# Optimization experiments

Measured on AMD Instinct MI355X. Metric: run time of the kernel, lower is better.

Reference implementation:

```python
import jax, jax.numpy as jnp
import numpy as np
from jax import lax

NUM_INPUTS = 1024
NUM_OUTPUTS = 1024
NUM_LAYERS = 32          # 1 first + (NUM_LAYERS-1) middle + 1 last, per torch __init__
N = 4096                 # num_neurons_per_layer
W = 65536                # parallel bit-array width


def _nand_layer(x, idx, mask):
    # x: [num_in, W] bool; idx: [num_out, 2] int; mask: [num_out] bool
    g = x[idx]                       # [num_out, 2, W] gather
    out = g[:, 0, :] & g[:, 1, :]    # bitwise AND
    return jnp.where(mask[:, None], ~out, out)  # conditional NOT


def setup_inputs() -> dict:
    key = jax.random.key(0)
    k = jax.random.split(key, 7)
    n_mid = NUM_LAYERS - 1
    return {
        "input_bitarrays": jax.random.bernoulli(k[0], 0.5, (NUM_INPUTS, W)),
        "idx_first": jax.random.randint(k[1], (N, 2), 0, NUM_INPUTS, dtype=jnp.int64 if jax.config.jax_enable_x64 else jnp.int32),
        "mask_first": jax.random.bernoulli(k[2], 0.5, (N,)),
        "idx_mid": jax.random.randint(k[3], (n_mid, N, 2), 0, N, dtype=jnp.int64 if jax.config.jax_enable_x64 else jnp.int32),
        "mask_mid": jax.random.bernoulli(k[4], 0.5, (n_mid, N)),
        "idx_last": jax.random.randint(k[5], (NUM_OUTPUTS, 2), 0, N, dtype=jnp.int64 if jax.config.jax_enable_x64 else jnp.int32),
        "mask_last": jax.random.bernoulli(k[6], 0.5, (NUM_OUTPUTS,)),
    }


def reference(input_bitarrays, idx_first, mask_first, idx_mid, mask_mid, idx_last, mask_last):
    x = _nand_layer(input_bitarrays, idx_first, mask_first)

    def step(carry, params):
        idx, mask = params
        return _nand_layer(carry, idx, mask), None

    x, _ = lax.scan(step, x, (idx_mid, mask_mid))
    return _nand_layer(x, idx_last, mask_last)
```

## Files before the change

### kernel.cpp

```cpp
#include <hip/hip_runtime.h>
#include <stdint.h>

#define NINPUTS   1024
#define NOUTPUTS  1024
#define NMID      31
#define NN        4096
#define W         65536
#define CHUNK     128
#define WPN       4
#define NCHUNKS   (W / CHUNK)
#define GRID      256
#define CPW       (NCHUNKS / GRID)
#define THREADS   1024
#define NPAIRS    16
#define TBL_BYTES ((size_t)NPAIRS * NN * 16)

__global__ void build_tbl_kernel(const int*      __restrict__ idx_first,
                                 const uint32_t* __restrict__ mask_first,
                                 const int*      __restrict__ idx_mid,
                                 const uint32_t* __restrict__ mask_mid,
                                 uint4*          __restrict__ tbl)
{
    const int tid = blockIdx.x * blockDim.x + threadIdx.x;
    const int F = tid >> 12;
    const int n = tid & (NN - 1);

    const int*      i1;
    const uint32_t* m1;
    if (F == 0) { i1 = idx_first; m1 = mask_first; }
    else        { i1 = idx_mid + (size_t)(2 * F - 1) * NN * 2;
                  m1 = mask_mid + (size_t)(2 * F - 1) * NN; }
    const int*      i2 = idx_mid + (size_t)(2 * F) * NN * 2;
    const uint32_t* m2 = mask_mid + (size_t)(2 * F) * NN;

    const int j = i2[2 * n];
    const int k = i2[2 * n + 1];
    uint4 e;
    e.x = (uint32_t)(i1[2 * j]     * 16) | (m1[j] ? 0x80000000u : 0u);
    e.y = (uint32_t)(i1[2 * j + 1] * 16);
    e.z = (uint32_t)(i1[2 * k]     * 16) | (m1[k] ? 0x80000000u : 0u);
    e.w = (uint32_t)(i1[2 * k + 1] * 16) | (m2[n] ? 0x80000000u : 0u);
    tbl[(size_t)F * NN + n] = e;
}

__global__ __launch_bounds__(THREADS, 4)
void nand_fused_kernel(const uint32_t* __restrict__ in,
                       const uint4*    __restrict__ tbl,
                       const int*      __restrict__ idx_last,
                       const uint32_t* __restrict__ mask_last,
                       uint32_t*       __restrict__ out)
{
    __shared__ uint32_t lds[40960];
    uint32_t* P = lds;
    uint32_t* X = lds + 4096;
    uint32_t* Y = lds + 20480;
    uint32_t* R = lds + 36864;

    const int t      = threadIdx.x;
    const int l      = t & 63;
    const int wv     = t >> 6;
    const int lane32 = l & 31;
    const int half   = l >> 5;
    const int shift  = half ? 32 : 0;
    const int bcol   = blockIdx.x * (CPW * CHUNK);

    #pragma unroll 4
    for (int s = 0; s < 32; ++s) {
        const int r = s * 32 + wv * 2 + half;
        const uint4 v = *(const uint4*)(in + (size_t)r * W + bcol + lane32 * 4);
        const unsigned long long b0 = __ballot(v.x != 0u);
        const unsigned long long b1 = __ballot(v.y != 0u);
        const unsigned long long b2 = __ballot(v.z != 0u);
        const unsigned long long b3 = __ballot(v.w != 0u);
        if (lane32 == 0) {
            uint4 w;
            w.x = (uint32_t)(b0 >> shift);
            w.y = (uint32_t)(b1 >> shift);
            w.z = (uint32_t)(b2 >> shift);
            w.w = (uint32_t)(b3 >> shift);
            *(uint4*)&P[r * WPN] = w;
        }
    }
    __syncthreads();

    for (int i = 0; i < CPW; ++i) {
        const int c0n = bcol + (i + 1) * CHUNK;
        const int c0p = bcol + (i - 1) * CHUNK;
        const bool do_pack   = (i + 1 < CPW);
        const bool do_unpack = (i > 0);

        uint4 tc[4], tn[4];
        #pragma unroll
        for (int k = 0; k < 4; ++k) tc[k] = tbl[k * THREADS + t];

        for (int F = 0; F <= 16; ++F) {
            uint4 pv0 = {0,0,0,0}, pv1 = {0,0,0,0};
            int pr0 = 0, pr1 = 0;
            if (do_pack && F >= 1) {
                pr0 = (F - 1) * 64 + wv * 2 + half;
                pr1 = pr0 + 32;
                pv0 = *(const uint4*)(in + (size_t)pr0 * W + c0n + lane32 * 4);
                pv1 = *(const uint4*)(in + (size_t)pr1 * W + c0n + lane32 * 4);
            }
            if (F <= 14) {
                #pragma unroll
                for (int k = 0; k < 4; ++k)
                    tn[k] = tbl[(size_t)(F + 1) * NN + k * THREADS + t];
            }

            if (F <= 15) {
                const uint32_t* src = (F == 0) ? P : ((F & 1) ? X : Y);
                uint32_t*       dst = (F & 1) ? Y : X;
                #pragma unroll
                for (int k = 0; k < 4; ++k) {
                    const int n = k * THREADS + t;
                    const uint4 e = tc[k];
                    const uint32_t xm1 = (uint32_t)((int32_t)e.x >> 31);
                    const uint32_t xm2 = (uint32_t)((int32_t)e.z >> 31);
                    const uint32_t xm3 = (uint32_t)((int32_t)e.w >> 31);
                    const uint4 a = *(const uint4*)((const char*)src + (e.x & 0xFFFFu));
                    const uint4 b = *(const uint4*)((const char*)src + e.y);
                    const uint4 c = *(const uint4*)((const char*)src + (e.z & 0xFFFFu));
                    const uint4 d = *(const uint4*)((const char*)src + (e.w & 0xFFFFu));
                    uint4 r;
                    r.x = (((a.x & b.x) ^ xm1) & ((c.x & d.x) ^ xm2)) ^ xm3;
                    r.y = (((a.y & b.y) ^ xm1) & ((c.y & d.y) ^ xm2)) ^ xm3;
                    r.z = (((a.z & b.z) ^ xm1) & ((c.z & d.z) ^ xm2)) ^ xm3;
                    r.w = (((a.w & b.w) ^ xm1) & ((c.w & d.w) ^ xm2)) ^ xm3;
                    *(uint4*)&dst[n * WPN] = r;
                }
            } else {
                const int n = t;
                const int2 ij = ((const int2*)idx_last)[n];
                const uint32_t xm = mask_last[n] ? 0xFFFFFFFFu : 0u;
                const uint4 a = *(const uint4*)&Y[ij.x * WPN];
                const uint4 b = *(const uint4*)&Y[ij.y * WPN];
                uint4 r;
                r.x = (a.x & b.x) ^ xm;  r.y = (a.y & b.y) ^ xm;
                r.z = (a.z & b.z) ^ xm;  r.w = (a.w & b.w) ^ xm;
                *(uint4*)&R[n * WPN] = r;
            }

            if (do_unpack && F <= 15) {
                #pragma unroll
                for (int s = 0; s < 2; ++s) {
                    const int r = F * 64 + s * 32 + wv * 2 + half;
                    const uint4 w4 = *(const uint4*)&R[r * WPN];
                    uint4 v;
                    v.x = (w4.x >> lane32) & 1u;
                    v.y = (w4.y >> lane32) & 1u;
                    v.z = (w4.z >> lane32) & 1u;
                    v.w = (w4.w >> lane32) & 1u;
                    *(uint4*)(out + (size_t)r * W + c0p + lane32 * 4) = v;
                }
            }

            if (do_pack && F >= 1) {
                {
                    const unsigned long long b0 = __ballot(pv0.x != 0u);
                    const unsigned long long b1 = __ballot(pv0.y != 0u);
                    const unsigned long long b2 = __ballot(pv0.z != 0u);
                    const unsigned long long b3 = __ballot(pv0.w != 0u);
                    if (lane32 == 0) {
                        uint4 w;
                        w.x = (uint32_t)(b0 >> shift);
                        w.y = (uint32_t)(b1 >> shift);
                        w.z = (uint32_t)(b2 >> shift);
                        w.w = (uint32_t)(b3 >> shift);
                        *(uint4*)&P[pr0 * WPN] = w;
                    }
                }
                {
                    const unsigned long long b0 = __ballot(pv1.x != 0u);
                    const unsigned long long b1 = __ballot(pv1.y != 0u);
                    const unsigned long long b2 = __ballot(pv1.z != 0u);
                    const unsigned long long b3 = __ballot(pv1.w != 0u);
                    if (lane32 == 0) {
                        uint4 w;
                        w.x = (uint32_t)(b0 >> shift);
                        w.y = (uint32_t)(b1 >> shift);
                        w.z = (uint32_t)(b2 >> shift);
                        w.w = (uint32_t)(b3 >> shift);
                        *(uint4*)&P[pr1 * WPN] = w;
                    }
                }
            }

            if (F <= 14) {
                #pragma unroll
                for (int k = 0; k < 4; ++k) tc[k] = tn[k];
            }
            __syncthreads();
        }
    }

    {
        const int c0l = bcol + (CPW - 1) * CHUNK;
        #pragma unroll 4
        for (int s = 0; s < 32; ++s) {
            const int r = s * 32 + wv * 2 + half;
            const uint4 w4 = *(const uint4*)&R[r * WPN];
            uint4 v;
            v.x = (w4.x >> lane32) & 1u;
            v.y = (w4.y >> lane32) & 1u;
            v.z = (w4.z >> lane32) & 1u;
            v.w = (w4.w >> lane32) & 1u;
            *(uint4*)(out + (size_t)r * W + c0l + lane32 * 4) = v;
        }
    }
}

__global__ __launch_bounds__(THREADS, 4)
void nand_pipe128_kernel(const uint32_t* __restrict__ in,
                         const int*      __restrict__ idx_first,
                         const uint32_t* __restrict__ mask_first,
                         const int*      __restrict__ idx_mid,
                         const uint32_t* __restrict__ mask_mid,
                         const int*      __restrict__ idx_last,
                         const uint32_t* __restrict__ mask_last,
                         uint32_t*       __restrict__ out)
{
    __shared__ uint32_t lds[40960];
    uint32_t* P = lds;
    uint32_t* X = lds + 4096;
    uint32_t* Y = lds + 20480;
    uint32_t* R = lds + 36864;

    const int t      = threadIdx.x;
    const int l      = t & 63;
    const int wv     = t >> 6;
    const int lane32 = l & 31;
    const int half   = l >> 5;
    const int shift  = half ? 32 : 0;
    const int bcol   = blockIdx.x * (CPW * CHUNK);

    #pragma unroll 4
    for (int s = 0; s < 32; ++s) {
        const int r = s * 32 + wv * 2 + half;
        const uint4 v = *(const uint4*)(in + (size_t)r * W + bcol + lane32 * 4);
        const unsigned long long b0 = __ballot(v.x != 0u);
        const unsigned long long b1 = __ballot(v.y != 0u);
        const unsigned long long b2 = __ballot(v.z != 0u);
        const unsigned long long b3 = __ballot(v.w != 0u);
        if (lane32 == 0) {
            uint4 w;
            w.x = (uint32_t)(b0 >> shift);  w.y = (uint32_t)(b1 >> shift);
            w.z = (uint32_t)(b2 >> shift);  w.w = (uint32_t)(b3 >> shift);
            *(uint4*)&P[r * WPN] = w;
        }
    }
    __syncthreads();

    for (int i = 0; i < CPW; ++i) {
        const int c0n = bcol + (i + 1) * CHUNK;
        const int c0p = bcol + (i - 1) * CHUNK;
        const bool do_pack   = (i + 1 < CPW);
        const bool do_unpack = (i > 0);

        for (int L = 0; L <= 32; ++L) {
            uint4 pv = {0, 0, 0, 0};
            int   pr = 0;
            if (do_pack && L >= 1) {
                pr = (L - 1) * 32 + wv * 2 + half;
                pv = *(const uint4*)(in + (size_t)pr * W + c0n + lane32 * 4);
            }
            if (L == 0) {
                #pragma unroll
                for (int k = 0; k < NN / THREADS; ++k) {
                    const int n = k * THREADS + t;
                    const int2 ij = ((const int2*)idx_first)[n];
                    const uint32_t xm = mask_first[n] ? 0xFFFFFFFFu : 0u;
                    const uint4 a = *(const uint4*)&P[ij.x * WPN];
                    const uint4 b = *(const uint4*)&P[ij.y * WPN];
                    uint4 r;
                    r.x = (a.x & b.x) ^ xm;  r.y = (a.y & b.y) ^ xm;
                    r.z = (a.z & b.z) ^ xm;  r.w = (a.w & b.w) ^ xm;
                    *(uint4*)&X[n * WPN] = r;
                }
            } else if (L <= 31) {
                const int*      idxL = idx_mid + (size_t)(L - 1) * NN * 2;
                const uint32_t* mL   = mask_mid + (size_t)(L - 1) * NN;
                const uint32_t* src  = (L & 1) ? X : Y;
                uint32_t*       dst  = (L & 1) ? Y : X;
                #pragma unroll
                for (int k = 0; k < NN / THREADS; ++k) {
                    const int n = k * THREADS + t;
                    const int2 ij = ((const int2*)idxL)[n];
                    const uint32_t xm = mL[n] ? 0xFFFFFFFFu : 0u;
                    const uint4 a = *(const uint4*)&src[ij.x * WPN];
                    const uint4 b = *(const uint4*)&src[ij.y * WPN];
                    uint4 r;
                    r.x = (a.x & b.x) ^ xm;  r.y = (a.y & b.y) ^ xm;
                    r.z = (a.z & b.z) ^ xm;  r.w = (a.w & b.w) ^ xm;
                    *(uint4*)&dst[n * WPN] = r;
                }
            } else {
                const int n = t;
                const int2 ij = ((const int2*)idx_last)[n];
                const uint32_t xm = mask_last[n] ? 0xFFFFFFFFu : 0u;
                const uint4 a = *(const uint4*)&Y[ij.x * WPN];
                const uint4 b = *(const uint4*)&Y[ij.y * WPN];
                uint4 r;
                r.x = (a.x & b.x) ^ xm;  r.y = (a.y & b.y) ^ xm;
                r.z = (a.z & b.z) ^ xm;  r.w = (a.w & b.w) ^ xm;
                *(uint4*)&R[n * WPN] = r;
            }
            if (do_unpack && L <= 31) {
                const int r = L * 32 + wv * 2 + half;
                const uint4 w4 = *(const uint4*)&R[r * WPN];
                uint4 v;
                v.x = (w4.x >> lane32) & 1u;  v.y = (w4.y >> lane32) & 1u;
                v.z = (w4.z >> lane32) & 1u;  v.w = (w4.w >> lane32) & 1u;
                *(uint4*)(out + (size_t)r * W + c0p + lane32 * 4) = v;
            }
            if (do_pack && L >= 1) {
                const unsigned long long b0 = __ballot(pv.x != 0u);
                const unsigned long long b1 = __ballot(pv.y != 0u);
                const unsigned long long b2 = __ballot(pv.z != 0u);
                const unsigned long long b3 = __ballot(pv.w != 0u);
                if (lane32 == 0) {
                    uint4 w;
                    w.x = (uint32_t)(b0 >> shift);  w.y = (uint32_t)(b1 >> shift);
                    w.z = (uint32_t)(b2 >> shift);  w.w = (uint32_t)(b3 >> shift);
                    *(uint4*)&P[pr * WPN] = w;
                }
            }
            __syncthreads();
        }
    }
    {
        const int c0l = bcol + (CPW - 1) * CHUNK;
        #pragma unroll 4
        for (int s = 0; s < 32; ++s) {
            const int r = s * 32 + wv * 2 + half;
            const uint4 w4 = *(const uint4*)&R[r * WPN];
            uint4 v;
            v.x = (w4.x >> lane32) & 1u;  v.y = (w4.y >> lane32) & 1u;
            v.z = (w4.z >> lane32) & 1u;  v.w = (w4.w >> lane32) & 1u;
            *(uint4*)(out + (size_t)r * W + c0l + lane32 * 4) = v;
        }
    }
}

extern "C" void kernel_launch(void* const* d_in, const int* in_sizes, int n_in,
                              void* d_out, int out_size, void* d_ws, size_t ws_size,
                              hipStream_t stream) {
    const uint32_t* in         = (const uint32_t*)d_in[0];
    const int*      idx_first  = (const int*)d_in[1];
    const uint32_t* mask_first = (const uint32_t*)d_in[2];
    const int*      idx_mid    = (const int*)d_in[3];
    const uint32_t* mask_mid   = (const uint32_t*)d_in[4];
    const int*      idx_last   = (const int*)d_in[5];
    const uint32_t* mask_last  = (const uint32_t*)d_in[6];
    uint32_t*       out        = (uint32_t*)d_out;

    if (ws_size >= TBL_BYTES) {
        uint4* tbl = (uint4*)d_ws;
        build_tbl_kernel<<<(NPAIRS * NN) / 256, 256, 0, stream>>>(
            idx_first, mask_first, idx_mid, mask_mid, tbl);
        nand_fused_kernel<<<GRID, THREADS, 0, stream>>>(
            in, tbl, idx_last, mask_last, out);
    } else {
        nand_pipe128_kernel<<<GRID, THREADS, 0, stream>>>(
            in, idx_first, mask_first, idx_mid, mask_mid, idx_last, mask_last, out);
    }
}
```

Before: 158.5 us.

## Sort fused gate table by LDS bank key to cut bank conflicts

The table-building kernel now counting-sorts the fused two-layer gate entries within each layer pair. The sort key is built from the low address bits of the four source operands, and the entries are scattered so that each wavefront's lanes read LDS addresses in a bank-friendly pattern. Each entry now stores its destination offset and the three mask bits, so the main kernel writes results to a per-entry location rather than one derived from thread index. The aim is fewer LDS bank conflicts on the four gathered uint4 reads per gate. In exchange, table building runs on only 16 blocks with a histogram, a scan and atomics, and the scattered stores may themselves conflict.

```diff
diff --git a/kernel.cpp b/kernel.cpp
--- a/kernel.cpp
+++ b/kernel.cpp
@@ -15,15 +15,17 @@
 #define NPAIRS    16
 #define TBL_BYTES ((size_t)NPAIRS * NN * 16)
 
-__global__ void build_tbl_kernel(const int*      __restrict__ idx_first,
-                                 const uint32_t* __restrict__ mask_first,
-                                 const int*      __restrict__ idx_mid,
-                                 const uint32_t* __restrict__ mask_mid,
-                                 uint4*          __restrict__ tbl)
+__global__ __launch_bounds__(1024)
+void build_sorted_tbl_kernel(const int*      __restrict__ idx_first,
+                             const uint32_t* __restrict__ mask_first,
+                             const int*      __restrict__ idx_mid,
+                             const uint32_t* __restrict__ mask_mid,
+                             uint4*          __restrict__ tbl)
 {
-    const int tid = blockIdx.x * blockDim.x + threadIdx.x;
-    const int F = tid >> 12;
-    const int n = tid & (NN - 1);
+    __shared__ uint32_t hist[4096];
+    __shared__ uint32_t wsum[1024];
+    const int F = blockIdx.x;
+    const int t = threadIdx.x;
 
     const int*      i1;
     const uint32_t* m1;
@@ -33,14 +35,60 @@
     const int*      i2 = idx_mid + (size_t)(2 * F) * NN * 2;
     const uint32_t* m2 = mask_mid + (size_t)(2 * F) * NN;
 
-    const int j = i2[2 * n];
-    const int k = i2[2 * n + 1];
-    uint4 e;
-    e.x = (uint32_t)(i1[2 * j]     * 16) | (m1[j] ? 0x80000000u : 0u);
-    e.y = (uint32_t)(i1[2 * j + 1] * 16);
-    e.z = (uint32_t)(i1[2 * k]     * 16) | (m1[k] ? 0x80000000u : 0u);
-    e.w = (uint32_t)(i1[2 * k + 1] * 16) | (m2[n] ? 0x80000000u : 0u);
-    tbl[(size_t)F * NN + n] = e;
+    #pragma unroll
+    for (int k = 0; k < 4; ++k) hist[k * 1024 + t] = 0;
+    __syncthreads();
+
+    uint4    ent[4];
+    uint32_t key[4];
+    #pragma unroll
+    for (int k = 0; k < 4; ++k) {
+        const int n = k * 1024 + t;
+        const int j  = i2[2 * n];
+        const int kk = i2[2 * n + 1];
+        const uint32_t a1 = (uint32_t)i1[2 * j]      * 16u;
+        const uint32_t b1 = (uint32_t)i1[2 * j + 1]  * 16u;
+        const uint32_t a2 = (uint32_t)i1[2 * kk]     * 16u;
+        const uint32_t b2 = (uint32_t)i1[2 * kk + 1] * 16u;
+        uint32_t mz = (uint32_t)(n * 16);
+        if (m1[j])  mz |= 1u << 29;
+        if (m1[kk]) mz |= 1u << 30;
+        if (m2[n])  mz |= 1u << 31;
+        ent[k].x = a1 | (b1 << 16);
+        ent[k].y = a2 | (b2 << 16);
+        ent[k].z = mz;
+        ent[k].w = 0;
+        key[k] = (((a1 >> 4) & 7u) << 9) | (((b1 >> 4) & 7u) << 6) |
+                 (((a2 >> 4) & 7u) << 3) |  ((b2 >> 4) & 7u);
+        atomicAdd(&hist[key[k]], 1u);
+    }
+    __syncthreads();
+
+    const uint32_t l0 = hist[4 * t], l1 = hist[4 * t + 1];
+    const uint32_t l2 = hist[4 * t + 2], l3 = hist[4 * t + 3];
+    const uint32_t lsum = l0 + l1 + l2 + l3;
+    wsum[t] = lsum;
+    __syncthreads();
+    for (int off = 1; off < 1024; off <<= 1) {
+        const uint32_t v = (t >= off) ? wsum[t - off] : 0u;
+        __syncthreads();
+        wsum[t] += v;
+        __syncthreads();
+    }
+    const uint32_t excl = wsum[t] - lsum;
+    hist[4 * t]     = excl;
+    hist[4 * t + 1] = excl + l0;
+    hist[4 * t + 2] = excl + l0 + l1;
+    hist[4 * t + 3] = excl + l0 + l1 + l2;
+    __syncthreads();
+
+    #pragma unroll
+    for (int k = 0; k < 4; ++k) {
+        const uint32_t p  = atomicAdd(&hist[key[k]], 1u);
+        const uint32_t op = p & 63u;
+        const uint32_t idx = (op >> 4) * 1024u + (op & 15u) * 64u + (p >> 6);
+        tbl[(size_t)F * NN + idx] = ent[k];
+    }
 }
 
 __global__ __launch_bounds__(THREADS, 4)
@@ -113,21 +161,23 @@
                 uint32_t*       dst = (F & 1) ? Y : X;
                 #pragma unroll
                 for (int k = 0; k < 4; ++k) {
-                    const int n = k * THREADS + t;
                     const uint4 e = tc[k];
-                    const uint32_t xm1 = (uint32_t)((int32_t)e.x >> 31);
-                    const uint32_t xm2 = (uint32_t)((int32_t)e.z >> 31);
-                    const uint32_t xm3 = (uint32_t)((int32_t)e.w >> 31);
-                    const uint4 a = *(const uint4*)((const char*)src + (e.x & 0xFFFFu));
-                    const uint4 b = *(const uint4*)((const char*)src + e.y);
-                    const uint4 c = *(const uint4*)((const char*)src + (e.z & 0xFFFFu));
-                    const uint4 d = *(const uint4*)((const char*)src + (e.w & 0xFFFFu));
+                    const uint32_t a1 = e.x & 0xFFFFu, b1 = e.x >> 16;
+                    const uint32_t a2 = e.y & 0xFFFFu, b2 = e.y >> 16;
+                    const uint32_t d0 = e.z & 0xFFFFu;
+                    const uint32_t xm1 = (uint32_t)((int32_t)(e.z << 2) >> 31);
+                    const uint32_t xm2 = (uint32_t)((int32_t)(e.z << 1) >> 31);
+                    const uint32_t xm3 = (uint32_t)((int32_t)e.z >> 31);
+                    const uint4 a = *(const uint4*)((const char*)src + a1);
+                    const uint4 b = *(const uint4*)((const char*)src + b1);
+                    const uint4 c = *(const uint4*)((const char*)src + a2);
+                    const uint4 d = *(const uint4*)((const char*)src + b2);
                     uint4 r;
                     r.x = (((a.x & b.x) ^ xm1) & ((c.x & d.x) ^ xm2)) ^ xm3;
                     r.y = (((a.y & b.y) ^ xm1) & ((c.y & d.y) ^ xm2)) ^ xm3;
                     r.z = (((a.z & b.z) ^ xm1) & ((c.z & d.z) ^ xm2)) ^ xm3;
                     r.w = (((a.w & b.w) ^ xm1) & ((c.w & d.w) ^ xm2)) ^ xm3;
-                    *(uint4*)&dst[n * WPN] = r;
+                    *(uint4*)((char*)dst + d0) = r;
                 }
             } else {
                 const int n = t;
@@ -356,7 +406,7 @@
 
     if (ws_size >= TBL_BYTES) {
         uint4* tbl = (uint4*)d_ws;
-        build_tbl_kernel<<<(NPAIRS * NN) / 256, 256, 0, stream>>>(
+        build_sorted_tbl_kernel<<<NPAIRS, 1024, 0, stream>>>(
             idx_first, mask_first, idx_mid, mask_mid, tbl);
         nand_fused_kernel<<<GRID, THREADS, 0, stream>>>(
             in, tbl, idx_last, mask_last, out);
```

Result: slower. 183.4 us (+15.7%).
